# Kernel optimization log

Hardware: AMD Instinct MI355X
Metric: run time of the kernel (lower is better)

## Reference

```python
import jax, jax.numpy as jnp
import numpy as np

N = 50000          # num nodes
E = 800000         # num edges (before self-loops)
D = 256            # feature dim for all layers
C = 2              # num classes
SLOPE = 0.2        # GATConv default negative_slope


def setup_inputs() -> dict:
    key = jax.random.key(0)
    ks = jax.random.split(key, 14)
    s = 1.0 / np.sqrt(D)
    inp = {
        "x": jax.random.normal(ks[0], (N, D), dtype=jnp.float32),
        "edge_index": jax.random.randint(ks[1], (2, E), 0, N, dtype=jnp.int64),
        # GAT layer 1 (heads=1): lin weight, att_src, att_dst, bias
        "W1": jax.random.normal(ks[2], (D, D), dtype=jnp.float32) * s,
        "a1s": jax.random.normal(ks[3], (D,), dtype=jnp.float32) * s,
        "a1d": jax.random.normal(ks[4], (D,), dtype=jnp.float32) * s,
        "b1": jnp.zeros((D,), dtype=jnp.float32),
        # GAT layer 2
        "W2": jax.random.normal(ks[5], (D, D), dtype=jnp.float32) * s,
        "a2s": jax.random.normal(ks[6], (D,), dtype=jnp.float32) * s,
        "a2d": jax.random.normal(ks[7], (D,), dtype=jnp.float32) * s,
        "b2": jnp.zeros((D,), dtype=jnp.float32),
        # classifier
        "Wc": jax.random.normal(ks[8], (D, C), dtype=jnp.float32) * s,
        "bc": jnp.zeros((C,), dtype=jnp.float32),
    }
    return inp


def _gat_layer(x, src, dst, W, a_src, a_dst, b):
    """PyG GATConv (heads=1, concat=True) with self-loops already in src/dst."""
    h = x @ W                                   # [N, D] node GEMM
    es = h @ a_src                              # [N] per-node src attention term
    ed = h @ a_dst                              # [N]
    e = jax.nn.leaky_relu(es[src] + ed[dst], SLOPE)   # [E'] per-edge logit
    # segment softmax over incoming edges of each dst node
    m = jax.ops.segment_max(e, dst, num_segments=N)   # [N]
    ex = jnp.exp(e - m[dst])
    den = jax.ops.segment_sum(ex, dst, num_segments=N)
    alpha = ex / den[dst]                       # [E']
    # weighted scatter-aggregate of source features
    out = jax.ops.segment_sum(alpha[:, None] * h[src], dst, num_segments=N)
    return out + b


def reference(x, edge_index, W1, a1s, a1d, b1, W2, a2s, a2d, b2, Wc, bc):
    loops = jnp.arange(N, dtype=edge_index.dtype)
    src = jnp.concatenate([edge_index[0], loops])   # add_self_loops=True
    dst = jnp.concatenate([edge_index[1], loops])
    h = jax.nn.relu(_gat_layer(x, src, dst, W1, a1s, a1d, b1))
    h = jax.nn.relu(_gat_layer(h, src, dst, W2, a2s, a2d, b2))
    logits = h @ Wc + bc                        # [N, C]
    return jax.nn.log_softmax(logits, axis=1)
```

## Files before the change

### kernel.cpp

```cpp
#include <hip/hip_runtime.h>
#include <math.h>

#define N_NODES 50000
#define N_EDGES 800000
#define EP (N_EDGES + N_NODES)
#define D 256
#define SLOPE 0.2f
#define NBIN 196
#define BINB 6144
#define SORTA 208
#define SAE 4096
#define TWG 512
#define CASTG 12500
#define GEMMB 782

typedef __attribute__((ext_vector_type(8))) short short8;
typedef __attribute__((ext_vector_type(4))) float f32x4;
typedef const __attribute__((address_space(1))) unsigned int* as1_u32;
typedef __attribute__((address_space(3))) unsigned int* as3_u32;

__device__ __forceinline__ unsigned short f2b(float f) {
    unsigned u = __float_as_uint(f);
    unsigned r = (u + 0x7FFFu + ((u >> 16) & 1u)) >> 16;
    return (unsigned short)r;
}
__device__ __forceinline__ float uas(unsigned u) { return __uint_as_float(u); }
__device__ __forceinline__ void g2lds16(const void* g, void* l) {
    __builtin_amdgcn_global_load_lds((as1_u32)g, (as3_u32)l, 16, 0, 0);
}


__global__ __launch_bounds__(256) void prep0(const int* __restrict__ ei,
                                             const float* __restrict__ W1,
                                             const float* __restrict__ W2,
                                             const float* __restrict__ x,
                                             unsigned short* __restrict__ Wt1,
                                             unsigned short* __restrict__ Wt2,
                                             unsigned short* __restrict__ xb,
                                             int* __restrict__ binCnt,
                                             int* __restrict__ coarse) {
    __shared__ float t[16][17];
    __shared__ int hist[NBIN], base[NBIN], lrk[NBIN];
    int bid = blockIdx.x;
    if (bid < SORTA) {
        int e0 = bid * SAE;
        for (int i = threadIdx.x; i < NBIN; i += 256) { hist[i] = 0; lrk[i] = 0; }
        __syncthreads();
        for (int i = threadIdx.x; i < SAE; i += 256) {
            int k = e0 + i;
            if (k >= EP) break;
            int d = (k < N_EDGES) ? ei[N_EDGES + k] : (k - N_EDGES);
            atomicAdd(&hist[d >> 8], 1);
        }
        __syncthreads();
        for (int i = threadIdx.x; i < NBIN; i += 256)
            if (hist[i]) base[i] = atomicAdd(&binCnt[i], hist[i]);
        __syncthreads();
        for (int i = threadIdx.x; i < SAE; i += 256) {
            int k = e0 + i;
            if (k >= EP) break;
            int s, d;
            if (k < N_EDGES) { s = ei[k]; d = ei[N_EDGES + k]; }
            else             { s = d = k - N_EDGES; }
            int b = d >> 8;
            int r = base[b] + atomicAdd(&lrk[b], 1);
            if (r < BINB) coarse[b * BINB + r] = s | ((d & 255) << 16);
        }
    } else if (bid < SORTA + TWG) {
        int t2 = bid - SORTA;
        const float* W = (t2 < 256) ? W1 : W2;
        unsigned short* Wt = (t2 < 256) ? Wt1 : Wt2;
        int tile = t2 & 255;
        int bx = (tile & 15) * 16, by = (tile >> 4) * 16;
        int lx = threadIdx.x & 15, ly = threadIdx.x >> 4;
        t[ly][lx] = W[(bx + ly) * D + by + lx];
        __syncthreads();
        Wt[(by + ly) * D + bx + lx] = f2b(t[lx][ly]);
    } else {
        int i = (bid - SORTA - TWG) * 256 + threadIdx.x;
        float4 v = ((const float4*)x)[i];
        ushort4 o;
        o.x = f2b(v.x); o.y = f2b(v.y); o.z = f2b(v.z); o.w = f2b(v.w);
        ((ushort4*)xb)[i] = o;
    }
}


__global__ __launch_bounds__(1024) void sortB(const int* __restrict__ coarse,
                                              const int* __restrict__ binCnt,
                                              int* __restrict__ srcC,
                                              int2* __restrict__ rpc) {
    __shared__ int h[256], off[256], h2[256];
    __shared__ int ssrc[BINB];
    int bin = blockIdx.x, tid = threadIdx.x;
    int cnt = binCnt[bin];
    if (cnt > BINB) cnt = BINB;
    if (tid < 256) { h[tid] = 0; h2[tid] = 0; }
    __syncthreads();
    int vv[6]; int nv = 0;
#pragma unroll
    for (int it = 0; it < 6; ++it) {
        int i = it * 1024 + tid;
        if (i < cnt) {
            int v = coarse[bin * BINB + i];
            vv[nv++] = v;
            atomicAdd(&h[v >> 16], 1);
        }
    }
    __syncthreads();
    if (tid < 256) off[tid] = h[tid];
    __syncthreads();
    for (int o = 1; o < 256; o <<= 1) {
        int tv = (tid < 256 && tid >= o) ? off[tid - o] : 0;
        __syncthreads();
        if (tid < 256) off[tid] += tv;
        __syncthreads();
    }
    for (int j = 0; j < nv; ++j) {
        int ld = vv[j] >> 16;
        int pos = off[ld] - h[ld] + atomicAdd(&h2[ld], 1);
        ssrc[pos] = vv[j] & 0xffff;
    }
    __syncthreads();
#pragma unroll
    for (int it = 0; it < 6; ++it) {
        int i = it * 1024 + tid;
        if (i < cnt) srcC[bin * BINB + i] = ssrc[i];
    }
    int node = bin * 256 + tid;
    if (tid < 256 && node < N_NODES)
        rpc[node] = make_int2(bin * BINB + off[tid] - h[tid], h[tid]);
}


__global__ __launch_bounds__(256) void gemm_bf16(const short* __restrict__ A,
                                                 const short* __restrict__ Wt,
                                                 unsigned short* __restrict__ C,
                                                 const float* __restrict__ avs,
                                                 const float* __restrict__ avd,
                                                 float* __restrict__ esp,
                                                 float* __restrict__ edp) {
    __shared__ short sbuf[128 * 132];
    short* lA = sbuf;
    short* lB = sbuf + 128 * 64;
    int bid = blockIdx.x;
    int cb, y;
    if (bid < 768) { int g2 = bid >> 4, r = bid & 15; y = g2 * 8 + (r & 7); cb = r >> 3; }
    else           { int t = bid - 768; y = 384 + (t >> 1); cb = t & 1; }
    int row0 = y << 7;
    int col0 = cb << 7;
    int tid = threadIdx.x, wave = tid >> 6, lane = tid & 63;
    int q = lane >> 4, m = lane & 15;
    int lr = lane >> 3;
    int kseg = (lane & 7) ^ lr;

    f32x4 acc[2][8] = {};
    for (int kc = 0; kc < 4; ++kc) {
        if (kc) __syncthreads();
#pragma unroll
        for (int it = 0; it < 4; ++it) {
            int rl = wave * 32 + it * 8;
            int gr = row0 + rl + lr;
            if (gr >= N_NODES) gr = N_NODES - 1;
            g2lds16(A + (((size_t)gr) << 8) + kc * 64 + kseg * 8, &lA[rl * 64]);
            int gc = col0 + rl + lr;
            g2lds16(Wt + (((size_t)gc) << 8) + kc * 64 + kseg * 8, &lB[rl * 64]);
        }
        __syncthreads();
#pragma unroll
        for (int ks = 0; ks < 2; ++ks) {
            int sw = ((ks * 4 + q) ^ (m & 7)) * 8;
            short8 a0 = *(const short8*)&lA[(wave * 32 + m) * 64 + sw];
            short8 a1 = *(const short8*)&lA[(wave * 32 + 16 + m) * 64 + sw];
#pragma unroll
            for (int ct = 0; ct < 8; ++ct) {
                short8 bf = *(const short8*)&lB[(ct * 16 + m) * 64 + sw];
                acc[0][ct] = __builtin_amdgcn_mfma_f32_16x16x32_bf16(a0, bf, acc[0][ct], 0, 0, 0);
                acc[1][ct] = __builtin_amdgcn_mfma_f32_16x16x32_bf16(a1, bf, acc[1][ct], 0, 0, 0);
            }
        }
    }

    float asv[8], adv[8];
#pragma unroll
    for (int ct = 0; ct < 8; ++ct) {
        asv[ct] = avs[col0 + ct * 16 + m];
        adv[ct] = avd[col0 + ct * 16 + m];
    }
    float* esw = esp + (cb ? N_NODES : 0);
    float* edw = edp + (cb ? N_NODES : 0);
    int rbase = row0 + wave * 32;
#pragma unroll
    for (int rt = 0; rt < 2; ++rt) {
        float ps[4] = {0.f, 0.f, 0.f, 0.f};
        float pd[4] = {0.f, 0.f, 0.f, 0.f};
#pragma unroll
        for (int ct = 0; ct < 8; ++ct)
#pragma unroll
            for (int rr = 0; rr < 4; ++rr) {
                float v = acc[rt][ct][rr];
                ps[rr] += v * asv[ct];
                pd[rr] += v * adv[ct];
            }
#pragma unroll
        for (int rr = 0; rr < 4; ++rr) {
#pragma unroll
            for (int off = 1; off < 16; off <<= 1) {
                ps[rr] += __shfl_xor(ps[rr], off);
                pd[rr] += __shfl_xor(pd[rr], off);
            }
        }
        if (m == 0) {
#pragma unroll
            for (int rr = 0; rr < 4; ++rr) {
                int row = rbase + rt * 16 + q * 4 + rr;
                if (row < N_NODES) {
                    esw[row] = ps[rr];
                    edw[row] = pd[rr];
                }
            }
        }
    }

    __syncthreads();
#pragma unroll
    for (int rt = 0; rt < 2; ++rt)
#pragma unroll
        for (int ct = 0; ct < 8; ++ct)
#pragma unroll
            for (int rr = 0; rr < 4; ++rr) {
                int lrow = wave * 32 + rt * 16 + q * 4 + rr;
                sbuf[lrow * 132 + ct * 16 + m] = (short)f2b(acc[rt][ct][rr]);
            }
    __syncthreads();
#pragma unroll
    for (int it = 0; it < 8; ++it) {
        int idx = it * 256 + tid;
        int lrow = idx >> 4, cg = idx & 15;
        int row = row0 + lrow;
        if (row < N_NODES)
            *(short8*)&C[(((size_t)row) << 8) + col0 + cg * 8] = *(const short8*)&sbuf[lrow * 132 + cg * 8];
    }
}


template<int CLS>
__global__ __launch_bounds__(256) void aggregate(const unsigned short* __restrict__ h,
                                                 const float* __restrict__ esp,
                                                 const float* __restrict__ edp,
                                                 const int2* __restrict__ rpc,
                                                 const int* __restrict__ srcC,
                                                 const float* __restrict__ bias,
                                                 unsigned short* __restrict__ outg,
                                                 const float* __restrict__ Wc,
                                                 const float* __restrict__ bc,
                                                 float* __restrict__ out) {
    __shared__ float wbuf[4][64];
    __shared__ int   sbuf[4][64];
    int wv = threadIdx.x >> 6;
    int node = blockIdx.x * 4 + wv;
    if (node >= N_NODES) return;
    int lane = threadIdx.x & 63;
    int lane32 = lane & 31, half = lane >> 5;
    size_t fo = (size_t)lane32 * 8;
    int2 rc = rpc[node];
    int start = rc.x;
    int cnt = rc.y > 64 ? 64 : rc.y;
    float edn = edp[node] + edp[N_NODES + node];

    int s = node;
    float w = 0.f;
    if (lane < cnt) {
        s = srcC[start + lane];
        float e = esp[s] + esp[N_NODES + s] + edn;
        e = e > 0.f ? e : SLOPE * e;
        w = __expf(fminf(e, 80.f));
    }
    wbuf[wv][lane] = w;
    sbuf[wv][lane] = s;
    float den = w;
    float accf[8] = {};

#pragma unroll 8
    for (int jj = 0; jj < cnt; jj += 2) {
        int idx = jj + half;
        float wj = wbuf[wv][idx];
        int sj = sbuf[wv][idx];
        uint4 u = *(const uint4*)&h[(((size_t)sj) << 8) + fo];
        accf[0] += wj * uas(u.x << 16);
        accf[1] += wj * uas(u.x & 0xffff0000u);
        accf[2] += wj * uas(u.y << 16);
        accf[3] += wj * uas(u.y & 0xffff0000u);
        accf[4] += wj * uas(u.z << 16);
        accf[5] += wj * uas(u.z & 0xffff0000u);
        accf[6] += wj * uas(u.w << 16);
        accf[7] += wj * uas(u.w & 0xffff0000u);
    }
    for (int off = 32; off; off >>= 1) den += __shfl_xor(den, off);
#pragma unroll
    for (int i = 0; i < 8; ++i) accf[i] += __shfl_xor(accf[i], 32);

    float inv = 1.f / den;
    float4 b0 = *(const float4*)&bias[fo];
    float4 b1 = *(const float4*)&bias[fo + 4];
    float r[8];
    r[0] = fmaxf(accf[0] * inv + b0.x, 0.f);
    r[1] = fmaxf(accf[1] * inv + b0.y, 0.f);
    r[2] = fmaxf(accf[2] * inv + b0.z, 0.f);
    r[3] = fmaxf(accf[3] * inv + b0.w, 0.f);
    r[4] = fmaxf(accf[4] * inv + b1.x, 0.f);
    r[5] = fmaxf(accf[5] * inv + b1.y, 0.f);
    r[6] = fmaxf(accf[6] * inv + b1.z, 0.f);
    r[7] = fmaxf(accf[7] * inv + b1.w, 0.f);

    if (!CLS) {
        if (half == 0) {
            short8 o;
#pragma unroll
            for (int i = 0; i < 8; ++i) o[i] = (short)f2b(r[i]);
            *(short8*)&outg[(((size_t)node) << 8) + fo] = o;
        }
    } else {
        float l0 = 0.f, l1 = 0.f;
#pragma unroll
        for (int f2 = 0; f2 < 4; ++f2) {
            float4 wc = *(const float4*)&Wc[fo * 2 + f2 * 4];
            l0 += r[f2 * 2] * wc.x + r[f2 * 2 + 1] * wc.z;
            l1 += r[f2 * 2] * wc.y + r[f2 * 2 + 1] * wc.w;
        }
#pragma unroll
        for (int off = 1; off < 32; off <<= 1) {
            l0 += __shfl_xor(l0, off);
            l1 += __shfl_xor(l1, off);
        }
        if (lane == 0) {
            l0 += bc[0];
            l1 += bc[1];
            float mx = fmaxf(l0, l1);
            float z = logf(__expf(l0 - mx) + __expf(l1 - mx));
            out[node * 2 + 0] = l0 - mx - z;
            out[node * 2 + 1] = l1 - mx - z;
        }
    }
}


extern "C" void kernel_launch(void* const* d_in, const int* in_sizes, int n_in,
                              void* d_out, int out_size, void* d_ws, size_t ws_size,
                              hipStream_t stream) {
    const float* x   = (const float*)d_in[0];
    const int*   ei  = (const int*)d_in[1];
    const float* W1  = (const float*)d_in[2];
    const float* a1s = (const float*)d_in[3];
    const float* a1d = (const float*)d_in[4];
    const float* b1  = (const float*)d_in[5];
    const float* W2  = (const float*)d_in[6];
    const float* a2s = (const float*)d_in[7];
    const float* a2d = (const float*)d_in[8];
    const float* b2  = (const float*)d_in[9];
    const float* Wc  = (const float*)d_in[10];
    const float* bc  = (const float*)d_in[11];
    float* out = (float*)d_out;

    char* p = (char*)d_ws;
    unsigned short* xb  = (unsigned short*)p; p += (size_t)N_NODES * D * 2;
    unsigned short* h   = (unsigned short*)p; p += (size_t)N_NODES * D * 2;
    unsigned short* g   = (unsigned short*)p; p += (size_t)N_NODES * D * 2;
    unsigned short* Wt1 = (unsigned short*)p; p += (size_t)D * D * 2;
    unsigned short* Wt2 = (unsigned short*)p; p += (size_t)D * D * 2;
    int*  coarse = (int*)p;  p += (size_t)NBIN * BINB * 4;
    int*  srcC   = (int*)p;  p += (size_t)NBIN * BINB * 4;
    int2* rpc    = (int2*)p; p += (size_t)N_NODES * 8;
    float* esp   = (float*)p; p += (size_t)2 * N_NODES * 4;
    float* edp   = (float*)p; p += (size_t)2 * N_NODES * 4;
    int*  binCnt = (int*)p;  p += (size_t)NBIN * 4;

    hipMemsetAsync(binCnt, 0, (size_t)NBIN * 4, stream);

    dim3 b256(256);
    int ngrid = (N_NODES + 3) / 4;

    prep0<<<SORTA + TWG + CASTG, b256, 0, stream>>>(ei, W1, W2, x, Wt1, Wt2, xb, binCnt, coarse);
    sortB<<<NBIN, 1024, 0, stream>>>(coarse, binCnt, srcC, rpc);

    gemm_bf16<<<GEMMB, b256, 0, stream>>>((const short*)xb, (const short*)Wt1, h,
                                          a1s, a1d, esp, edp);
    aggregate<0><<<ngrid, b256, 0, stream>>>(h, esp, edp, rpc, srcC, b1, g,
                                             nullptr, nullptr, nullptr);
    gemm_bf16<<<GEMMB, b256, 0, stream>>>((const short*)g, (const short*)Wt2, h,
                                          a2s, a2d, esp, edp);
    aggregate<1><<<ngrid, b256, 0, stream>>>(h, esp, edp, rpc, srcC, b2, nullptr,
                                             Wc, bc, out);
}
```

Before: 308.6 us.

## Replace CSR sort kernel with fixed-capacity per-node buckets fused into GEMM launch

Drops the separate sortB kernel (histogram, prefix scan, local scatter) and instead has extra blocks appended to the first GEMM launch write each edge source straight into a fixed 64-slot bucket per destination node via shared-memory atomics. Aggregation then indexes srcC at node*64 and reads a plain count array. This removes a kernel launch and the scan work, and overlaps the bucketing with the GEMM. In exchange it uses a larger padded srcC array and gives up the contiguous CSR layout, so edge order within a node becomes nondeterministic.

```diff
diff --git a/kernel.cpp b/kernel.cpp
--- a/kernel.cpp
+++ b/kernel.cpp
@@ -13,6 +13,7 @@
 #define TWG 512
 #define CASTG 12500
 #define GEMMB 782
+#define CAP 64
 
 typedef __attribute__((ext_vector_type(8))) short short8;
 typedef __attribute__((ext_vector_type(4))) float f32x4;
@@ -86,64 +87,41 @@
 }
 
 
-__global__ __launch_bounds__(1024) void sortB(const int* __restrict__ coarse,
-                                              const int* __restrict__ binCnt,
-                                              int* __restrict__ srcC,
-                                              int2* __restrict__ rpc) {
-    __shared__ int h[256], off[256], h2[256];
-    __shared__ int ssrc[BINB];
-    int bin = blockIdx.x, tid = threadIdx.x;
-    int cnt = binCnt[bin];
-    if (cnt > BINB) cnt = BINB;
-    if (tid < 256) { h[tid] = 0; h2[tid] = 0; }
-    __syncthreads();
-    int vv[6]; int nv = 0;
-#pragma unroll
-    for (int it = 0; it < 6; ++it) {
-        int i = it * 1024 + tid;
-        if (i < cnt) {
-            int v = coarse[bin * BINB + i];
-            vv[nv++] = v;
-            atomicAdd(&h[v >> 16], 1);
-        }
-    }
-    __syncthreads();
-    if (tid < 256) off[tid] = h[tid];
-    __syncthreads();
-    for (int o = 1; o < 256; o <<= 1) {
-        int tv = (tid < 256 && tid >= o) ? off[tid - o] : 0;
-        __syncthreads();
-        if (tid < 256) off[tid] += tv;
-        __syncthreads();
-    }
-    for (int j = 0; j < nv; ++j) {
-        int ld = vv[j] >> 16;
-        int pos = off[ld] - h[ld] + atomicAdd(&h2[ld], 1);
-        ssrc[pos] = vv[j] & 0xffff;
-    }
-    __syncthreads();
-#pragma unroll
-    for (int it = 0; it < 6; ++it) {
-        int i = it * 1024 + tid;
-        if (i < cnt) srcC[bin * BINB + i] = ssrc[i];
-    }
-    int node = bin * 256 + tid;
-    if (tid < 256 && node < N_NODES)
-        rpc[node] = make_int2(bin * BINB + off[tid] - h[tid], h[tid]);
-}
-
-
+template<int SORT>
 __global__ __launch_bounds__(256) void gemm_bf16(const short* __restrict__ A,
                                                  const short* __restrict__ Wt,
                                                  unsigned short* __restrict__ C,
                                                  const float* __restrict__ avs,
                                                  const float* __restrict__ avd,
                                                  float* __restrict__ esp,
-                                                 float* __restrict__ edp) {
+                                                 float* __restrict__ edp,
+                                                 const int* __restrict__ coarse,
+                                                 const int* __restrict__ binCnt,
+                                                 int* __restrict__ srcC,
+                                                 int* __restrict__ cntN) {
     __shared__ short sbuf[128 * 132];
+    __shared__ int h2[256];
+    int bid = blockIdx.x;
+    if (SORT && bid >= GEMMB) {
+        int bin = bid - GEMMB;
+        int tid = threadIdx.x;
+        h2[tid] = 0;
+        int cb2 = binCnt[bin];
+        if (cb2 > BINB) cb2 = BINB;
+        __syncthreads();
+        for (int i = tid; i < cb2; i += 256) {
+            int v = coarse[bin * BINB + i];
+            int ld = v >> 16;
+            int pos = atomicAdd(&h2[ld], 1);
+            if (pos < CAP) srcC[((bin * 256 + ld) << 6) + pos] = v & 0xffff;
+        }
+        __syncthreads();
+        int node = bin * 256 + tid;
+        if (node < N_NODES) cntN[node] = h2[tid];
+        return;
+    }
     short* lA = sbuf;
     short* lB = sbuf + 128 * 64;
-    int bid = blockIdx.x;
     int cb, y;
     if (bid < 768) { int g2 = bid >> 4, r = bid & 15; y = g2 * 8 + (r & 7); cb = r >> 3; }
     else           { int t = bid - 768; y = 384 + (t >> 1); cb = t & 1; }
@@ -248,7 +226,7 @@
 __global__ __launch_bounds__(256) void aggregate(const unsigned short* __restrict__ h,
                                                  const float* __restrict__ esp,
                                                  const float* __restrict__ edp,
-                                                 const int2* __restrict__ rpc,
+                                                 const int* __restrict__ cntv,
                                                  const int* __restrict__ srcC,
                                                  const float* __restrict__ bias,
                                                  unsigned short* __restrict__ outg,
@@ -263,15 +241,14 @@
     int lane = threadIdx.x & 63;
     int lane32 = lane & 31, half = lane >> 5;
     size_t fo = (size_t)lane32 * 8;
-    int2 rc = rpc[node];
-    int start = rc.x;
-    int cnt = rc.y > 64 ? 64 : rc.y;
+    int cnt = cntv[node];
+    if (cnt > CAP) cnt = CAP;
     float edn = edp[node] + edp[N_NODES + node];
 
     int s = node;
     float w = 0.f;
     if (lane < cnt) {
-        s = srcC[start + lane];
+        s = srcC[(node << 6) + lane];
         float e = esp[s] + esp[N_NODES + s] + edn;
         e = e > 0.f ? e : SLOPE * e;
         w = __expf(fminf(e, 80.f));
@@ -369,8 +346,8 @@
     unsigned short* Wt1 = (unsigned short*)p; p += (size_t)D * D * 2;
     unsigned short* Wt2 = (unsigned short*)p; p += (size_t)D * D * 2;
     int*  coarse = (int*)p;  p += (size_t)NBIN * BINB * 4;
-    int*  srcC   = (int*)p;  p += (size_t)NBIN * BINB * 4;
-    int2* rpc    = (int2*)p; p += (size_t)N_NODES * 8;
+    int*  srcC   = (int*)p;  p += (size_t)N_NODES * CAP * 4;
+    int*  cntN   = (int*)p;  p += (size_t)N_NODES * 4;
     float* esp   = (float*)p; p += (size_t)2 * N_NODES * 4;
     float* edp   = (float*)p; p += (size_t)2 * N_NODES * 4;
     int*  binCnt = (int*)p;  p += (size_t)NBIN * 4;
@@ -381,14 +358,15 @@
     int ngrid = (N_NODES + 3) / 4;
 
     prep0<<<SORTA + TWG + CASTG, b256, 0, stream>>>(ei, W1, W2, x, Wt1, Wt2, xb, binCnt, coarse);
-    sortB<<<NBIN, 1024, 0, stream>>>(coarse, binCnt, srcC, rpc);
-
-    gemm_bf16<<<GEMMB, b256, 0, stream>>>((const short*)xb, (const short*)Wt1, h,
-                                          a1s, a1d, esp, edp);
-    aggregate<0><<<ngrid, b256, 0, stream>>>(h, esp, edp, rpc, srcC, b1, g,
+
+    gemm_bf16<1><<<GEMMB + NBIN, b256, 0, stream>>>((const short*)xb, (const short*)Wt1, h,
+                                                    a1s, a1d, esp, edp,
+                                                    coarse, binCnt, srcC, cntN);
+    aggregate<0><<<ngrid, b256, 0, stream>>>(h, esp, edp, cntN, srcC, b1, g,
                                              nullptr, nullptr, nullptr);
-    gemm_bf16<<<GEMMB, b256, 0, stream>>>((const short*)g, (const short*)Wt2, h,
-                                          a2s, a2d, esp, edp);
-    aggregate<1><<<ngrid, b256, 0, stream>>>(h, esp, edp, rpc, srcC, b2, nullptr,
+    gemm_bf16<0><<<GEMMB, b256, 0, stream>>>((const short*)g, (const short*)Wt2, h,
+                                             a2s, a2d, esp, edp,
+                                             nullptr, nullptr, nullptr, nullptr);
+    aggregate<1><<<ngrid, b256, 0, stream>>>(h, esp, edp, cntN, srcC, b2, nullptr,
                                              Wc, bc, out);
 }
```

New measurement: 296.4 us. 3.9% less time.
